# Optimization experiments

Measured on AMD Instinct MI355X. Metric: run time of the kernel, lower is better.

The kernel has to match this reference:

```python
import jax, jax.numpy as jnp
import numpy as np

N, E = 50000, 1250000
IN_DIM, H, C, EDGE_DIM = 128, 2, 32, 64
NEG_SLOPE = 0.2


def setup_inputs() -> dict:
    key = jax.random.key(0)
    ks = jax.random.split(key, 9)
    x = jax.random.normal(ks[0], (N, IN_DIM), dtype=jnp.float32)
    edge_index = jax.random.randint(ks[1], (2, E), 0, N, dtype=jnp.int64)
    edge_attr = jax.random.normal(ks[2], (E, EDGE_DIM), dtype=jnp.float32)
    # learned params (PyG GATConv: glorot-style scale)
    W = jax.random.normal(ks[3], (IN_DIM, H * C), dtype=jnp.float32) * (1.0 / np.sqrt(IN_DIM))
    W_edge = jax.random.normal(ks[4], (EDGE_DIM, H * C), dtype=jnp.float32) * (1.0 / np.sqrt(EDGE_DIM))
    att_src = jax.random.normal(ks[5], (H, C), dtype=jnp.float32) * (1.0 / np.sqrt(C))
    att_dst = jax.random.normal(ks[6], (H, C), dtype=jnp.float32) * (1.0 / np.sqrt(C))
    att_edge = jax.random.normal(ks[7], (H, C), dtype=jnp.float32) * (1.0 / np.sqrt(C))
    bias = jnp.zeros((H * C,), dtype=jnp.float32)
    return {"x": x, "edge_index": edge_index, "edge_attr": edge_attr,
            "W": W, "W_edge": W_edge, "att_src": att_src, "att_dst": att_dst,
            "att_edge": att_edge, "bias": bias}


def reference(x, edge_index, edge_attr, W, W_edge, att_src, att_dst, att_edge, bias):
    # IntraGraphAttention.forward: relu then GATConv(in, 32, heads=2, edge_dim=64)
    x = jax.nn.relu(x)
    src, dst = edge_index[0], edge_index[1]

    # PyG add_self_loops(fill_value='mean'): self-loop edge_attr = mean of
    # incoming edge attrs per node (zeros for isolated nodes).
    deg = jax.ops.segment_sum(jnp.ones((E,), jnp.float32), dst, num_segments=N)
    loop_attr = jax.ops.segment_sum(edge_attr, dst, num_segments=N) / jnp.maximum(deg, 1.0)[:, None]
    loop_idx = jnp.arange(N, dtype=src.dtype)
    src_f = jnp.concatenate([src, loop_idx])          # [E+N]
    dst_f = jnp.concatenate([dst, loop_idx])          # [E+N]
    eattr_f = jnp.concatenate([edge_attr, loop_attr])  # [E+N, 64]

    # node / edge projections
    h = (x @ W).reshape(N, H, C)                       # [N,H,C]
    a_src = jnp.einsum('nhc,hc->nh', h, att_src)       # [N,H]
    a_dst = jnp.einsum('nhc,hc->nh', h, att_dst)       # [N,H]
    e = (eattr_f @ W_edge).reshape(-1, H, C)           # [E+N,H,C]
    a_edge = jnp.einsum('ehc,hc->eh', e, att_edge)     # [E+N,H]

    # per-edge attention logits
    alpha = a_src[src_f] + a_dst[dst_f] + a_edge       # [E+N,H]
    alpha = jax.nn.leaky_relu(alpha, NEG_SLOPE)

    # segment softmax over destination neighborhoods
    amax = jax.ops.segment_max(alpha, dst_f, num_segments=N)  # [N,H]
    p = jnp.exp(alpha - amax[dst_f])
    denom = jax.ops.segment_sum(p, dst_f, num_segments=N)     # [N,H]
    alpha = p / (denom[dst_f] + 1e-16)

    # scatter-aggregate messages (dropout dp=0 -> identity)
    msg = h[src_f] * alpha[..., None]                   # [E+N,H,C]
    out = jax.ops.segment_sum(msg, dst_f, num_segments=N)     # [N,H,C]
    return out.reshape(N, H * C) + bias
```

## Files before the change

### kernel.cpp

```cpp
#include <hip/hip_runtime.h>

#define NEG 0.2f

__global__ void k_wke(const float* __restrict__ W_edge, const float* __restrict__ att_edge,
                      float* __restrict__ wke) {
    int t = threadIdx.x;
    int hh = t >> 6;
    int k  = t & 63;
    float s = 0.f;
#pragma unroll
    for (int c = 0; c < 32; ++c)
        s += W_edge[k * 64 + hh * 32 + c] * att_edge[hh * 32 + c];
    wke[hh * 64 + k] = s;
}

__global__ __launch_bounds__(256) void k_node(
    const float* __restrict__ x, const float* __restrict__ W,
    const float* __restrict__ att_src, const float* __restrict__ att_dst,
    float* __restrict__ hbuf, float* __restrict__ a_src, float* __restrict__ a_dst, int N) {
    __shared__ float Wl[128 * 64];
    __shared__ float xs[4 * 128];
    int t = threadIdx.x;
    for (int i = t; i < 128 * 64; i += 256) Wl[i] = W[i];
    int col = t & 63;
    int nl  = t >> 6;
    float asw = att_src[col];
    float adw = att_dst[col];
    int node0 = blockIdx.x * 64;
    __syncthreads();
    for (int it = 0; it < 16; ++it) {
        int nb = node0 + it * 4;
        __syncthreads();
        for (int j = t; j < 512; j += 256) {
            int nn = nb + (j >> 7);
            int k  = j & 127;
            xs[j] = (nn < N) ? fmaxf(x[(size_t)nn * 128 + k], 0.f) : 0.f;
        }
        __syncthreads();
        int n = nb + nl;
        float acc = 0.f;
#pragma unroll 8
        for (int k = 0; k < 128; ++k)
            acc = fmaf(xs[nl * 128 + k], Wl[k * 64 + col], acc);
        float vs = acc * asw, vd = acc * adw;
#pragma unroll
        for (int m = 1; m <= 16; m <<= 1) {
            vs += __shfl_xor(vs, m, 64);
            vd += __shfl_xor(vd, m, 64);
        }
        if (n < N) {
            hbuf[(size_t)n * 64 + col] = acc;
            if ((col & 31) == 0) {
                int hh = col >> 5;
                a_src[n * 2 + hh] = vs;
                a_dst[n * 2 + hh] = vd;
            }
        }
    }
}

__global__ __launch_bounds__(256) void k_hist(const int* __restrict__ dstI, int* __restrict__ count,
                                              long long E) {
    long long i0 = (long long)blockIdx.x * 256 + threadIdx.x;
    long long stride = (long long)gridDim.x * 256;
    for (long long i = i0; i < E; i += stride)
        atomicAdd(&count[dstI[i]], 1);
}

__global__ __launch_bounds__(256) void k_scan1(const int* __restrict__ cnt, int* __restrict__ offs,
                                               int* __restrict__ bsum, int N) {
    __shared__ int ts[256];
    int t = threadIdx.x, blk = blockIdx.x;
    int base = blk * 1024 + t * 4;
    int v[4], s = 0;
#pragma unroll
    for (int i = 0; i < 4; ++i) {
        int idx = base + i;
        v[i] = (idx < N) ? cnt[idx] : 0;
        s += v[i];
    }
    ts[t] = s;
    __syncthreads();
    for (int off = 1; off < 256; off <<= 1) {
        int y = (t >= off) ? ts[t - off] : 0;
        __syncthreads();
        ts[t] += y;
        __syncthreads();
    }
    int run = ts[t] - s;
#pragma unroll
    for (int i = 0; i < 4; ++i) {
        int idx = base + i;
        if (idx < N) offs[idx] = run;
        run += v[i];
    }
    if (t == 255) bsum[blk] = ts[255];
}

__global__ void k_scan2(int* __restrict__ bsum, int nb) {
    if (threadIdx.x == 0) {
        int run = 0;
        for (int i = 0; i < nb; ++i) { int v = bsum[i]; bsum[i] = run; run += v; }
    }
}

__global__ void k_scan3(int* __restrict__ offs, const int* __restrict__ bsum,
                        int* __restrict__ cursor, int N) {
    int idx = blockIdx.x * 256 + threadIdx.x;
    if (idx < N) {
        int o = offs[idx] + bsum[idx >> 10];
        offs[idx] = o;
        cursor[idx] = o;
    }
}

__global__ __launch_bounds__(256) void k_pa(
    const float* __restrict__ edge_attr, const int* __restrict__ srcI,
    const int* __restrict__ dstI, const float* __restrict__ wke,
    int* __restrict__ cursor, int* __restrict__ srcperm, float2* __restrict__ paperm,
    long long E, int nwaves_total) {
    int lane = threadIdx.x & 63;
    int sub  = lane & 15;
    int grp  = lane >> 4;
    long long wave = (long long)blockIdx.x * 4 + (threadIdx.x >> 6);
    float w0[4], w1[4];
#pragma unroll
    for (int j = 0; j < 4; ++j) {
        w0[j] = wke[sub * 4 + j];
        w1[j] = wke[64 + sub * 4 + j];
    }
    for (long long base = wave * 4; base < E; base += (long long)nwaves_total * 4) {
        long long e = base + grp;
        bool valid = e < E;
        float pa0 = 0.f, pa1 = 0.f;
        if (valid) {
            const float4 ea = *(const float4*)(edge_attr + e * 64 + sub * 4);
            pa0 = ea.x * w0[0] + ea.y * w0[1] + ea.z * w0[2] + ea.w * w0[3];
            pa1 = ea.x * w1[0] + ea.y * w1[1] + ea.z * w1[2] + ea.w * w1[3];
        }
#pragma unroll
        for (int m = 1; m <= 8; m <<= 1) {
            pa0 += __shfl_xor(pa0, m, 64);
            pa1 += __shfl_xor(pa1, m, 64);
        }
        if (valid && sub == 0) {
            int s = srcI[e], d = dstI[e];
            int pos = atomicAdd(&cursor[d], 1);
            srcperm[pos] = s;
            paperm[pos] = make_float2(pa0, pa1);
        }
    }
}

__global__ __launch_bounds__(256) void k_agg(
    const int* __restrict__ srcperm, const float2* __restrict__ paperm,
    const int* __restrict__ offs, const int* __restrict__ count,
    const float* __restrict__ a_src, const float* __restrict__ a_dst,
    const float* __restrict__ hbuf, const float* __restrict__ bias,
    float* __restrict__ out, int N) {
    int t = threadIdx.x;
    int sub = t & 15;
    int n = blockIdx.x * 16 + (t >> 4);
    if (n >= N) return;
    int cnt  = count[n];
    int base = offs[n];
    float ad0 = a_dst[n * 2 + 0], ad1 = a_dst[n * 2 + 1];
    float accx = 0.f, accy = 0.f, accz = 0.f, accw = 0.f;
    float den0 = 0.f, den1 = 0.f, sae0 = 0.f, sae1 = 0.f;

    int   sj  = (cnt > 0) ? srcperm[base] : 0;
    float2 paj = (cnt > 0) ? paperm[base] : make_float2(0.f, 0.f);
    for (int j = 0; j < cnt; ++j) {
        int   snext  = (j + 1 < cnt) ? srcperm[base + j + 1] : 0;
        float2 panext = (j + 1 < cnt) ? paperm[base + j + 1] : make_float2(0.f, 0.f);
        float as0 = a_src[sj * 2 + 0], as1 = a_src[sj * 2 + 1];
        float l0 = as0 + ad0 + paj.x; l0 = l0 > 0.f ? l0 : NEG * l0;
        float l1 = as1 + ad1 + paj.y; l1 = l1 > 0.f ? l1 : NEG * l1;
        float q0 = __expf(l0), q1 = __expf(l1);
        const float4 hv = *(const float4*)(hbuf + (size_t)sj * 64 + sub * 4);
        float q = (sub < 8) ? q0 : q1;
        accx = fmaf(q, hv.x, accx);
        accy = fmaf(q, hv.y, accy);
        accz = fmaf(q, hv.z, accz);
        accw = fmaf(q, hv.w, accw);
        den0 += q0; den1 += q1;
        sae0 += paj.x; sae1 += paj.y;
        sj = snext; paj = panext;
    }
    float dg = (cnt > 0) ? (float)cnt : 1.f;
    float l0 = a_src[n * 2 + 0] + ad0 + sae0 / dg; l0 = l0 > 0.f ? l0 : NEG * l0;
    float l1 = a_src[n * 2 + 1] + ad1 + sae1 / dg; l1 = l1 > 0.f ? l1 : NEG * l1;
    float pl0 = __expf(l0), pl1 = __expf(l1);
    const float4 hn = *(const float4*)(hbuf + (size_t)n * 64 + sub * 4);
    float pl  = (sub < 8) ? pl0 : pl1;
    float den = ((sub < 8) ? den0 + pl0 : den1 + pl1) + 1e-16f;
    const float4 bv = *(const float4*)(bias + sub * 4);
    float4 o;
    o.x = (accx + pl * hn.x) / den + bv.x;
    o.y = (accy + pl * hn.y) / den + bv.y;
    o.z = (accz + pl * hn.z) / den + bv.z;
    o.w = (accw + pl * hn.w) / den + bv.w;
    *(float4*)(out + (size_t)n * 64 + sub * 4) = o;
}

extern "C" void kernel_launch(void* const* d_in, const int* in_sizes, int n_in,
                              void* d_out, int out_size, void* d_ws, size_t ws_size,
                              hipStream_t stream) {
    const float* x         = (const float*)d_in[0];
    const int*   ei        = (const int*)d_in[1];
    const float* edge_attr = (const float*)d_in[2];
    const float* W         = (const float*)d_in[3];
    const float* W_edge    = (const float*)d_in[4];
    const float* att_src   = (const float*)d_in[5];
    const float* att_dst   = (const float*)d_in[6];
    const float* att_edge  = (const float*)d_in[7];
    const float* bias      = (const float*)d_in[8];

    int N = in_sizes[0] / 128;
    long long E = in_sizes[1] / 2;
    const int* srcI = ei;
    const int* dstI = ei + E;

    char* ws = (char*)d_ws;
    float* wke     = (float*)ws;                      ws += 128 * 4;
    float* hbuf    = (float*)ws;                      ws += (size_t)N * 64 * 4;
    float* a_src   = (float*)ws;                      ws += (size_t)N * 2 * 4;
    float* a_dst   = (float*)ws;                      ws += (size_t)N * 2 * 4;
    float2* paperm = (float2*)ws;                     ws += (size_t)E * 2 * 4;
    int*   srcperm = (int*)ws;                        ws += (size_t)E * 4;
    int*   count   = (int*)ws;                        ws += (size_t)N * 4;
    int*   offs    = (int*)ws;                        ws += (size_t)N * 4;
    int*   cursor  = (int*)ws;                        ws += (size_t)N * 4;
    int*   bsum    = (int*)ws;                        ws += 64 * 4;

    hipMemsetAsync(count, 0, (size_t)N * sizeof(int), stream);

    k_wke<<<1, 128, 0, stream>>>(W_edge, att_edge, wke);
    k_node<<<(N + 63) / 64, 256, 0, stream>>>(x, W, att_src, att_dst, hbuf, a_src, a_dst, N);
    k_hist<<<2048, 256, 0, stream>>>(dstI, count, E);

    int nb = (N + 1023) / 1024;
    k_scan1<<<nb, 256, 0, stream>>>(count, offs, bsum, N);
    k_scan2<<<1, 64, 0, stream>>>(bsum, nb);
    k_scan3<<<(N + 255) / 256, 256, 0, stream>>>(offs, bsum, cursor, N);

    int nblocks = 2048;
    k_pa<<<nblocks, 256, 0, stream>>>(edge_attr, srcI, dstI, wke, cursor, srcperm, paperm,
                                      E, nblocks * 4);

    k_agg<<<(N + 15) / 16, 256, 0, stream>>>(srcperm, paperm, offs, count, a_src, a_dst,
                                             hbuf, bias, (float*)d_out, N);
}
```

Measured before the change: 310.2 us.

## Parallelize per-node aggregation across four edge groups, pack edge records, fuse wke

Result: faster. 291.2 us (-6.1%).

```diff
diff --git a/kernel.cpp b/kernel.cpp
--- a/kernel.cpp
+++ b/kernel.cpp
@@ -1,18 +1,6 @@
 #include <hip/hip_runtime.h>
 
 #define NEG 0.2f
-
-__global__ void k_wke(const float* __restrict__ W_edge, const float* __restrict__ att_edge,
-                      float* __restrict__ wke) {
-    int t = threadIdx.x;
-    int hh = t >> 6;
-    int k  = t & 63;
-    float s = 0.f;
-#pragma unroll
-    for (int c = 0; c < 32; ++c)
-        s += W_edge[k * 64 + hh * 32 + c] * att_edge[hh * 32 + c];
-    wke[hh * 64 + k] = s;
-}
 
 __global__ __launch_bounds__(256) void k_node(
     const float* __restrict__ x, const float* __restrict__ W,
@@ -59,8 +47,19 @@
     }
 }
 
-__global__ __launch_bounds__(256) void k_hist(const int* __restrict__ dstI, int* __restrict__ count,
-                                              long long E) {
+__global__ __launch_bounds__(256) void k_hist(
+    const int* __restrict__ dstI, int* __restrict__ count, long long E,
+    const float* __restrict__ W_edge, const float* __restrict__ att_edge,
+    float* __restrict__ wke) {
+    if (blockIdx.x == 0 && threadIdx.x < 128) {
+        int hh = threadIdx.x >> 6;
+        int k  = threadIdx.x & 63;
+        float s = 0.f;
+#pragma unroll
+        for (int c = 0; c < 32; ++c)
+            s += W_edge[k * 64 + hh * 32 + c] * att_edge[hh * 32 + c];
+        wke[hh * 64 + k] = s;
+    }
     long long i0 = (long long)blockIdx.x * 256 + threadIdx.x;
     long long stride = (long long)gridDim.x * 256;
     for (long long i = i0; i < E; i += stride)
@@ -98,10 +97,15 @@
 }
 
 __global__ void k_scan2(int* __restrict__ bsum, int nb) {
-    if (threadIdx.x == 0) {
-        int run = 0;
-        for (int i = 0; i < nb; ++i) { int v = bsum[i]; bsum[i] = run; run += v; }
-    }
+    int t = threadIdx.x;
+    int orig = (t < nb) ? bsum[t] : 0;
+    int v = orig;
+#pragma unroll
+    for (int off = 1; off < 64; off <<= 1) {
+        int y = __shfl_up(v, off, 64);
+        if (t >= off) v += y;
+    }
+    if (t < nb) bsum[t] = v - orig;
 }
 
 __global__ void k_scan3(int* __restrict__ offs, const int* __restrict__ bsum,
@@ -117,7 +121,7 @@
 __global__ __launch_bounds__(256) void k_pa(
     const float* __restrict__ edge_attr, const int* __restrict__ srcI,
     const int* __restrict__ dstI, const float* __restrict__ wke,
-    int* __restrict__ cursor, int* __restrict__ srcperm, float2* __restrict__ paperm,
+    int* __restrict__ cursor, float4* __restrict__ evec,
     long long E, int nwaves_total) {
     int lane = threadIdx.x & 63;
     int sub  = lane & 15;
@@ -146,21 +150,21 @@
         if (valid && sub == 0) {
             int s = srcI[e], d = dstI[e];
             int pos = atomicAdd(&cursor[d], 1);
-            srcperm[pos] = s;
-            paperm[pos] = make_float2(pa0, pa1);
+            evec[pos] = make_float4(pa0, pa1, __int_as_float(s), 0.f);
         }
     }
 }
 
 __global__ __launch_bounds__(256) void k_agg(
-    const int* __restrict__ srcperm, const float2* __restrict__ paperm,
-    const int* __restrict__ offs, const int* __restrict__ count,
-    const float* __restrict__ a_src, const float* __restrict__ a_dst,
-    const float* __restrict__ hbuf, const float* __restrict__ bias,
-    float* __restrict__ out, int N) {
+    const float4* __restrict__ evec, const int* __restrict__ offs,
+    const int* __restrict__ count, const float* __restrict__ a_src,
+    const float* __restrict__ a_dst, const float* __restrict__ hbuf,
+    const float* __restrict__ bias, float* __restrict__ out, int N) {
     int t = threadIdx.x;
-    int sub = t & 15;
-    int n = blockIdx.x * 16 + (t >> 4);
+    int lane = t & 63;
+    int sub = lane & 15;
+    int grp = lane >> 4;
+    int n = blockIdx.x * 4 + (t >> 6);
     if (n >= N) return;
     int cnt  = count[n];
     int base = offs[n];
@@ -168,39 +172,55 @@
     float accx = 0.f, accy = 0.f, accz = 0.f, accw = 0.f;
     float den0 = 0.f, den1 = 0.f, sae0 = 0.f, sae1 = 0.f;
 
-    int   sj  = (cnt > 0) ? srcperm[base] : 0;
-    float2 paj = (cnt > 0) ? paperm[base] : make_float2(0.f, 0.f);
-    for (int j = 0; j < cnt; ++j) {
-        int   snext  = (j + 1 < cnt) ? srcperm[base + j + 1] : 0;
-        float2 panext = (j + 1 < cnt) ? paperm[base + j + 1] : make_float2(0.f, 0.f);
-        float as0 = a_src[sj * 2 + 0], as1 = a_src[sj * 2 + 1];
-        float l0 = as0 + ad0 + paj.x; l0 = l0 > 0.f ? l0 : NEG * l0;
-        float l1 = as1 + ad1 + paj.y; l1 = l1 > 0.f ? l1 : NEG * l1;
-        float q0 = __expf(l0), q1 = __expf(l1);
-        const float4 hv = *(const float4*)(hbuf + (size_t)sj * 64 + sub * 4);
-        float q = (sub < 8) ? q0 : q1;
-        accx = fmaf(q, hv.x, accx);
-        accy = fmaf(q, hv.y, accy);
-        accz = fmaf(q, hv.z, accz);
-        accw = fmaf(q, hv.w, accw);
-        den0 += q0; den1 += q1;
-        sae0 += paj.x; sae1 += paj.y;
-        sj = snext; paj = panext;
-    }
+    if (cnt > 0) {
+        int last = cnt - 1;
+        float4 evA = evec[base + (grp < cnt ? grp : last)];
+        float4 evB = evec[base + (grp + 4 < cnt ? grp + 4 : last)];
+        int sA = __float_as_int(evA.z);
+        int sB = __float_as_int(evB.z);
+        float2 asA = *(const float2*)(a_src + 2 * (size_t)sA);
+        float4 hvA = *(const float4*)(hbuf + (size_t)sA * 64 + sub * 4);
+        for (int j = grp; j < cnt; j += 4) {
+            int jc = j + 8 < cnt ? j + 8 : last;
+            float4 evC = evec[base + jc];
+            float2 asB = *(const float2*)(a_src + 2 * (size_t)sB);
+            float4 hvB = *(const float4*)(hbuf + (size_t)sB * 64 + sub * 4);
+            float l0 = asA.x + ad0 + evA.x; l0 = l0 > 0.f ? l0 : NEG * l0;
+            float l1 = asA.y + ad1 + evA.y; l1 = l1 > 0.f ? l1 : NEG * l1;
+            float q0 = __expf(l0), q1 = __expf(l1);
+            float q = (sub < 8) ? q0 : q1;
+            accx = fmaf(q, hvA.x, accx);
+            accy = fmaf(q, hvA.y, accy);
+            accz = fmaf(q, hvA.z, accz);
+            accw = fmaf(q, hvA.w, accw);
+            den0 += q0; den1 += q1;
+            sae0 += evA.x; sae1 += evA.y;
+            evA = evB; sA = sB; asA = asB; hvA = hvB;
+            evB = evC; sB = __float_as_int(evC.z);
+        }
+    }
+#define RED2(v) { v += __shfl_xor(v, 16, 64); v += __shfl_xor(v, 32, 64); }
+    RED2(accx) RED2(accy) RED2(accz) RED2(accw)
+    RED2(den0) RED2(den1) RED2(sae0) RED2(sae1)
+#undef RED2
+
     float dg = (cnt > 0) ? (float)cnt : 1.f;
-    float l0 = a_src[n * 2 + 0] + ad0 + sae0 / dg; l0 = l0 > 0.f ? l0 : NEG * l0;
-    float l1 = a_src[n * 2 + 1] + ad1 + sae1 / dg; l1 = l1 > 0.f ? l1 : NEG * l1;
+    float as0 = a_src[n * 2 + 0], as1 = a_src[n * 2 + 1];
+    float l0 = as0 + ad0 + sae0 / dg; l0 = l0 > 0.f ? l0 : NEG * l0;
+    float l1 = as1 + ad1 + sae1 / dg; l1 = l1 > 0.f ? l1 : NEG * l1;
     float pl0 = __expf(l0), pl1 = __expf(l1);
     const float4 hn = *(const float4*)(hbuf + (size_t)n * 64 + sub * 4);
     float pl  = (sub < 8) ? pl0 : pl1;
     float den = ((sub < 8) ? den0 + pl0 : den1 + pl1) + 1e-16f;
     const float4 bv = *(const float4*)(bias + sub * 4);
-    float4 o;
-    o.x = (accx + pl * hn.x) / den + bv.x;
-    o.y = (accy + pl * hn.y) / den + bv.y;
-    o.z = (accz + pl * hn.z) / den + bv.z;
-    o.w = (accw + pl * hn.w) / den + bv.w;
-    *(float4*)(out + (size_t)n * 64 + sub * 4) = o;
+    if (grp == 0) {
+        float4 o;
+        o.x = (accx + pl * hn.x) / den + bv.x;
+        o.y = (accy + pl * hn.y) / den + bv.y;
+        o.z = (accz + pl * hn.z) / den + bv.z;
+        o.w = (accw + pl * hn.w) / den + bv.w;
+        *(float4*)(out + (size_t)n * 64 + sub * 4) = o;
+    }
 }
 
 extern "C" void kernel_launch(void* const* d_in, const int* in_sizes, int n_in,
@@ -222,22 +242,20 @@
     const int* dstI = ei + E;
 
     char* ws = (char*)d_ws;
-    float* wke     = (float*)ws;                      ws += 128 * 4;
-    float* hbuf    = (float*)ws;                      ws += (size_t)N * 64 * 4;
-    float* a_src   = (float*)ws;                      ws += (size_t)N * 2 * 4;
-    float* a_dst   = (float*)ws;                      ws += (size_t)N * 2 * 4;
-    float2* paperm = (float2*)ws;                     ws += (size_t)E * 2 * 4;
-    int*   srcperm = (int*)ws;                        ws += (size_t)E * 4;
-    int*   count   = (int*)ws;                        ws += (size_t)N * 4;
-    int*   offs    = (int*)ws;                        ws += (size_t)N * 4;
-    int*   cursor  = (int*)ws;                        ws += (size_t)N * 4;
-    int*   bsum    = (int*)ws;                        ws += 64 * 4;
+    float4* evec  = (float4*)ws;                      ws += (size_t)E * 16;
+    float* wke    = (float*)ws;                       ws += 128 * 4;
+    float* hbuf   = (float*)ws;                       ws += (size_t)N * 64 * 4;
+    float* a_src  = (float*)ws;                       ws += (size_t)N * 2 * 4;
+    float* a_dst  = (float*)ws;                       ws += (size_t)N * 2 * 4;
+    int*   count  = (int*)ws;                         ws += (size_t)N * 4;
+    int*   offs   = (int*)ws;                         ws += (size_t)N * 4;
+    int*   cursor = (int*)ws;                         ws += (size_t)N * 4;
+    int*   bsum   = (int*)ws;                         ws += 64 * 4;
 
     hipMemsetAsync(count, 0, (size_t)N * sizeof(int), stream);
 
-    k_wke<<<1, 128, 0, stream>>>(W_edge, att_edge, wke);
     k_node<<<(N + 63) / 64, 256, 0, stream>>>(x, W, att_src, att_dst, hbuf, a_src, a_dst, N);
-    k_hist<<<2048, 256, 0, stream>>>(dstI, count, E);
+    k_hist<<<2048, 256, 0, stream>>>(dstI, count, E, W_edge, att_edge, wke);
 
     int nb = (N + 1023) / 1024;
     k_scan1<<<nb, 256, 0, stream>>>(count, offs, bsum, N);
@@ -245,9 +263,8 @@
     k_scan3<<<(N + 255) / 256, 256, 0, stream>>>(offs, bsum, cursor, N);
 
     int nblocks = 2048;
-    k_pa<<<nblocks, 256, 0, stream>>>(edge_attr, srcI, dstI, wke, cursor, srcperm, paperm,
-                                      E, nblocks * 4);
-
-    k_agg<<<(N + 15) / 16, 256, 0, stream>>>(srcperm, paperm, offs, count, a_src, a_dst,
-                                             hbuf, bias, (float*)d_out, N);
-}
+    k_pa<<<nblocks, 256, 0, stream>>>(edge_attr, srcI, dstI, wke, cursor, evec, E, nblocks * 4);
+
+    k_agg<<<(N + 3) / 4, 256, 0, stream>>>(evec, offs, count, a_src, a_dst, hbuf, bias,
+                                           (float*)d_out, N);
+}
```
